# Kernel optimization log

Measured on AMD Instinct MI355X. Metric: run time of the kernel, lower is better.

## Reference

```python
import jax, jax.numpy as jnp
import numpy as np

B, C, H, W = 32, 384, 28, 28
E, HID, K = 4, 384, 2  # HID = hidden_features(1536) // num_experts(4)


def setup_inputs() -> dict:
    key = jax.random.key(0)
    ks = jax.random.split(key, 5)
    x = jax.random.normal(ks[0], (B, C, H, W), jnp.float32)
    gate_w = jax.random.normal(ks[1], (C, E), jnp.float32) * 0.02
    gate_b = jnp.zeros((E,), jnp.float32)
    w1 = jax.random.normal(ks[2], (E, HID, C), jnp.float32) * 0.02
    b1 = jnp.zeros((E, HID), jnp.float32)
    w2 = jax.random.normal(ks[3], (E, C, HID), jnp.float32) * 0.02
    b2 = jnp.zeros((E, C), jnp.float32)
    return {"x": x, "gate_w": gate_w, "gate_b": gate_b,
            "w1": w1, "b1": b1, "w2": w2, "b2": b2}


def reference(x, gate_w, gate_b, w1, b1, w2, b2):
    b, c, h, w = x.shape
    e = gate_b.shape[0]
    # per-token gating: tokens are spatial positions in NHWC order
    x_flat = x.transpose(0, 2, 3, 1).reshape(-1, c)          # [N, C], N = B*H*W
    scores = jax.nn.softmax(x_flat @ gate_w + gate_b, -1)    # [N, E]
    top_v, top_i = jax.lax.top_k(scores, K)                  # [N, K]
    top_w = jax.nn.softmax(top_v, -1)                        # [N, K] renormalized
    # weight map per top-k slot: [K, B, H, W]
    wmap = top_w.T.reshape(K, b, h, w)
    # faithful to torch loop: expert i contributes at slot k iff ANY token routed
    # to it at slot k; the weight applied is the UNMASKED slot-k weight map.
    present = (top_i[:, :, None] == jnp.arange(e)[None, None, :]).any(0)  # [K, E]
    coef = jnp.einsum('ke,kbhw->ebhw', present.astype(x.dtype), wmap)     # [E, B, H, W]
    # dense per-expert 1x1-conv MLP over the FULL tensor (as in the source)
    hdn = jax.nn.relu(jnp.einsum('bchw,edc->ebdhw', x, w1)
                      + b1[:, None, :, None, None])          # [E, B, HID, H, W]
    y = jnp.einsum('ebdhw,eod->ebohw', hdn, w2) + b2[:, None, :, None, None]
    out = jnp.einsum('ebohw,ebhw->bohw', y, coef)            # [B, C, H, W]
    return out
```

## Files before the change

### kernel.cpp

```cpp
#include <hip/hip_runtime.h>
#include <hip/hip_bf16.h>
#include <stdint.h>

#define B_DIM 32
#define C_DIM 384
#define HW_DIM 784
#define E_DIM 4
#define HID_DIM 384
#define NTOK (B_DIM * HW_DIM)
#define NH (E_DIM * HID_DIM)

using short8 = __attribute__((ext_vector_type(8))) short;
using f32x4  = __attribute__((ext_vector_type(4))) float;
typedef unsigned short ushort_t;

__device__ __forceinline__ ushort_t f2bf(float f) {
  __hip_bfloat16 h = __float2bfloat16(f);
  return __builtin_bit_cast(ushort_t, h);
}

__device__ __forceinline__ void gload_lds16(const void* g, void* l) {
  __builtin_amdgcn_global_load_lds(
      (const __attribute__((address_space(1))) unsigned int*)g,
      (__attribute__((address_space(3))) unsigned int*)l, 16, 0, 0);
}

__global__ __launch_bounds__(256) void prep_kernel(
    const float* __restrict__ w1, const float* __restrict__ w2,
    ushort_t* __restrict__ W1b, ushort_t* __restrict__ W2b,
    unsigned int* __restrict__ present) {
  int i = blockIdx.x * 256 + threadIdx.x;
  if (i == 0) *present = 0u;
  if (i < NH * C_DIM) {
    W1b[i] = f2bf(w1[i]);
    int o = i / NH;
    int r = i - o * NH;
    int e = r / HID_DIM;
    int k = r - e * HID_DIM;
    W2b[i] = f2bf(w2[((size_t)e * C_DIM + o) * HID_DIM + k]);
  }
}

__global__ __launch_bounds__(256) void gate_kernel(
    const float* __restrict__ x, const float* __restrict__ gw,
    const float* __restrict__ gb, ushort_t* __restrict__ xb,
    float* __restrict__ topw, unsigned int* __restrict__ present) {
  __shared__ __align__(16) ushort_t lxs[64][392];
  __shared__ float pscore[4][64][4];
  __shared__ unsigned int pmask;
  const int b = blockIdx.x;
  const int p0 = blockIdx.y * 64;
  const int cnt = min(64, HW_DIM - p0);
  const int tid = threadIdx.x;
  const int cg = tid >> 6, tl = tid & 63;
  if (tid == 0) pmask = 0u;
  float a0 = 0.f, a1 = 0.f, a2 = 0.f, a3 = 0.f;
  const bool valid = tl < cnt;
  if (valid) {
    const float* xp = x + (size_t)b * C_DIM * HW_DIM + p0 + tl;
    for (int c = cg; c < C_DIM; c += 4) {
      const float v = xp[(size_t)c * HW_DIM];
      lxs[tl][c] = f2bf(v);
      const float4 g = *(const float4*)&gw[c * 4];
      a0 += v * g.x; a1 += v * g.y; a2 += v * g.z; a3 += v * g.w;
    }
  }
  pscore[cg][tl][0] = a0; pscore[cg][tl][1] = a1;
  pscore[cg][tl][2] = a2; pscore[cg][tl][3] = a3;
  __syncthreads();
  if (cg == 0 && valid) {
    float z[4];
#pragma unroll
    for (int e = 0; e < 4; e++)
      z[e] = pscore[0][tl][e] + pscore[1][tl][e] + pscore[2][tl][e] +
             pscore[3][tl][e] + gb[e];
    const float mx = fmaxf(fmaxf(z[0], z[1]), fmaxf(z[2], z[3]));
    float s[4]; float sum = 0.f;
#pragma unroll
    for (int e = 0; e < 4; e++) { s[e] = __expf(z[e] - mx); sum += s[e]; }
    const float inv = 1.f / sum;
#pragma unroll
    for (int e = 0; e < 4; e++) s[e] *= inv;
    int e0 = 0; float v0 = s[0];
#pragma unroll
    for (int e = 1; e < 4; e++) if (s[e] > v0) { v0 = s[e]; e0 = e; }
    int e1 = -1; float v1 = -1.f;
#pragma unroll
    for (int e = 0; e < 4; e++) if (e != e0 && s[e] > v1) { v1 = s[e]; e1 = e; }
    const float r = __expf(v1 - v0);
    const float w0 = 1.f / (1.f + r);
    const int m = b * HW_DIM + p0 + tl;
    topw[m * 2] = w0;
    topw[m * 2 + 1] = 1.f - w0;
    atomicOr(&pmask, (1u << e0) | (1u << (4 + e1)));
  }
  __syncthreads();
  if (tid == 0) atomicOr(present, pmask);
  const int nchunk = cnt * 48;
  for (int ci = tid; ci < nchunk; ci += 256) {
    const int row = ci / 48, c8 = ci - row * 48;
    short8 v = *(const short8*)&lxs[row][c8 * 8];
    *(short8*)&xb[(size_t)(b * HW_DIM + p0 + row) * C_DIM + c8 * 8] = v;
  }
}

template <int KDIM, int EPI>
__global__ __launch_bounds__(256, 2) void gemm128(
    const ushort_t* __restrict__ A, const ushort_t* __restrict__ Bw,
    const float* __restrict__ bias, const float* __restrict__ topw,
    const unsigned int* __restrict__ presentp,
    ushort_t* __restrict__ hOut, float* __restrict__ outp) {
  constexpr int BM = 128, BN = 128, BK = 64;
  constexpr int KT = KDIM / BK;
  constexpr int NTN = (EPI == 0 ? NH / BN : C_DIM / BN);
  constexpr int ASZ = BM * BK;
  __shared__ ushort_t smem[4 * ASZ];

  const int nwg = NTN * (NTOK / BM);
  const int orig = blockIdx.x;
  const int xcd = orig & 7;
  const int qq = nwg >> 3, rr = nwg & 7;
  const int wg = (xcd < rr ? xcd * (qq + 1) : rr * (qq + 1) + (xcd - rr) * qq)
               + (orig >> 3);
  const int mt = wg / NTN, nt = wg % NTN;
  const int m0 = mt * BM, n0 = nt * BN;

  const int tid = threadIdx.x;
  const int lane = tid & 63;
  const int wid = tid >> 6;
  const int wm = wid >> 1, wn = wid & 1;

  auto stage = [&](int t) {
    ushort_t* dstA = smem + (t & 1) * ASZ;
    ushort_t* dstB = smem + 2 * ASZ + (t & 1) * ASZ;
    const int kb = t * BK;
#pragma unroll
    for (int li = 0; li < 4; ++li) {
      const int P = (li * 256 + tid) * 16;
      const int row = P >> 7;
      const int cb = (P & 127) ^ ((row & 7) << 4);
      gload_lds16(&A[(size_t)(m0 + row) * KDIM + kb + (cb >> 1)],
                  (char*)dstA + P);
    }
#pragma unroll
    for (int li = 0; li < 4; ++li) {
      const int P = (li * 256 + tid) * 16;
      const int row = P >> 7;
      const int cb = (P & 127) ^ ((row & 7) << 4);
      gload_lds16(&Bw[(size_t)(n0 + row) * KDIM + kb + (cb >> 1)],
                  (char*)dstB + P);
    }
  };

  f32x4 acc[4][4] = {};

  stage(0);
  stage(1);
  for (int t = 0; t < KT; ++t) {
    if (t + 1 < KT)
      asm volatile("s_waitcnt vmcnt(8)" ::: "memory");
    else
      asm volatile("s_waitcnt vmcnt(0)" ::: "memory");
    __builtin_amdgcn_sched_barrier(0);
    __builtin_amdgcn_s_barrier();
    __builtin_amdgcn_sched_barrier(0);
    const char* Ab = (const char*)(smem + (t & 1) * ASZ);
    const char* Bb = (const char*)(smem + 2 * ASZ + (t & 1) * ASZ);
    short8 av[4][2], bv[4][2];
#pragma unroll
    for (int i = 0; i < 4; ++i)
#pragma unroll
      for (int kk = 0; kk < 2; ++kk) {
        const int row = wm * 64 + i * 16 + (lane & 15);
        const int cb = (kk * 64 + ((lane >> 4) * 16)) ^ ((row & 7) << 4);
        av[i][kk] = *(const short8*)(Ab + row * 128 + cb);
      }
#pragma unroll
    for (int i = 0; i < 4; ++i)
#pragma unroll
      for (int kk = 0; kk < 2; ++kk) {
        const int row = wn * 64 + i * 16 + (lane & 15);
        const int cb = (kk * 64 + ((lane >> 4) * 16)) ^ ((row & 7) << 4);
        bv[i][kk] = *(const short8*)(Bb + row * 128 + cb);
      }
    __builtin_amdgcn_s_setprio(1);
#pragma unroll
    for (int kk = 0; kk < 2; ++kk)
#pragma unroll
      for (int i = 0; i < 4; ++i)
#pragma unroll
        for (int j = 0; j < 4; ++j)
          acc[i][j] = __builtin_amdgcn_mfma_f32_16x16x32_bf16(
              av[i][kk], bv[j][kk], acc[i][j], 0, 0, 0);
    __builtin_amdgcn_s_setprio(0);
    __builtin_amdgcn_sched_barrier(0);
    __builtin_amdgcn_s_barrier();
    __builtin_amdgcn_sched_barrier(0);
    if (t + 2 < KT) stage(t + 2);
  }

  const unsigned int pm = *presentp;
  if constexpr (EPI == 0) {
    ushort_t* tr = smem;
    const int e = n0 / HID_DIM;
    const float P0 = (float)((pm >> e) & 1u);
    const float P1 = (float)((pm >> (4 + e)) & 1u);
#pragma unroll
    for (int mi = 0; mi < 4; ++mi) {
      const int r0 = wm * 64 + mi * 16 + (lane >> 4) * 4;
      const int mg = m0 + r0;
      const float4 t0 = *(const float4*)&topw[mg * 2];
      const float4 t1 = *(const float4*)&topw[mg * 2 + 4];
      const float cj[4] = {P0 * t0.x + P1 * t0.y, P0 * t0.z + P1 * t0.w,
                           P0 * t1.x + P1 * t1.y, P0 * t1.z + P1 * t1.w};
#pragma unroll
      for (int ni = 0; ni < 4; ++ni) {
        const int cl = wn * 64 + ni * 16 + (lane & 15);
        const float bvv = bias[n0 + cl];
#pragma unroll
        for (int j = 0; j < 4; ++j) {
          float v = fmaxf(acc[mi][ni][j] + bvv, 0.f);
          tr[(r0 + j) * 128 + cl] = f2bf(cj[j] * v);
        }
      }
    }
    __syncthreads();
#pragma unroll
    for (int it = 0; it < 8; ++it) {
      const int c = it * 256 + tid;
      const int row = c >> 4, cr = c & 15;
      *(short8*)&hOut[(size_t)(m0 + row) * NH + n0 + cr * 8] =
          *(const short8*)&tr[row * 128 + cr * 8];
    }
  } else {
    float B0[4], B1[4];
#pragma unroll
    for (int ni = 0; ni < 4; ++ni) {
      const int o = n0 + wn * 64 + ni * 16 + (lane & 15);
      float s0 = 0.f, s1 = 0.f;
#pragma unroll
      for (int e2 = 0; e2 < 4; ++e2) {
        const float bb = bias[e2 * C_DIM + o];
        s0 += (float)((pm >> e2) & 1u) * bb;
        s1 += (float)((pm >> (4 + e2)) & 1u) * bb;
      }
      B0[ni] = s0; B1[ni] = s1;
    }
#pragma unroll
    for (int mi = 0; mi < 4; ++mi) {
      const int mg = m0 + wm * 64 + mi * 16 + (lane >> 4) * 4;
      const float4 t0 = *(const float4*)&topw[mg * 2];
      const float4 t1 = *(const float4*)&topw[mg * 2 + 4];
      const int bb2 = mg / HW_DIM;
      const int p = mg - bb2 * HW_DIM;
#pragma unroll
      for (int ni = 0; ni < 4; ++ni) {
        const int o = n0 + wn * 64 + ni * 16 + (lane & 15);
        float4 v;
        v.x = acc[mi][ni][0] + t0.x * B0[ni] + t0.y * B1[ni];
        v.y = acc[mi][ni][1] + t0.z * B0[ni] + t0.w * B1[ni];
        v.z = acc[mi][ni][2] + t1.x * B0[ni] + t1.y * B1[ni];
        v.w = acc[mi][ni][3] + t1.z * B0[ni] + t1.w * B1[ni];
        *(float4*)&outp[((size_t)bb2 * C_DIM + o) * HW_DIM + p] = v;
      }
    }
  }
}

extern "C" void kernel_launch(void* const* d_in, const int* in_sizes, int n_in,
                              void* d_out, int out_size, void* d_ws, size_t ws_size,
                              hipStream_t stream) {
  const float* x  = (const float*)d_in[0];
  const float* gw = (const float*)d_in[1];
  const float* gb = (const float*)d_in[2];
  const float* w1 = (const float*)d_in[3];
  const float* b1 = (const float*)d_in[4];
  const float* w2 = (const float*)d_in[5];
  const float* b2 = (const float*)d_in[6];
  float* out = (float*)d_out;

  char* ws = (char*)d_ws;
  ushort_t* xb = (ushort_t*)ws;   ws += (size_t)NTOK * C_DIM * 2;
  ushort_t* hdnS = (ushort_t*)ws; ws += (size_t)NTOK * NH * 2;
  ushort_t* W1b = (ushort_t*)ws;  ws += (size_t)NH * C_DIM * 2;
  ushort_t* W2b = (ushort_t*)ws;  ws += (size_t)C_DIM * NH * 2;
  float* topw = (float*)ws;       ws += (size_t)NTOK * 2 * 4;
  unsigned int* present = (unsigned int*)ws;

  prep_kernel<<<dim3((NH * C_DIM) / 256), dim3(256), 0, stream>>>(
      w1, w2, W1b, W2b, present);
  gate_kernel<<<dim3(B_DIM, 13), dim3(256), 0, stream>>>(
      x, gw, gb, xb, topw, present);
  gemm128<C_DIM, 0><<<dim3((NTOK / 128) * (NH / 128)), dim3(256), 0, stream>>>(
      xb, W1b, b1, topw, present, hdnS, nullptr);
  gemm128<NH, 1><<<dim3((NTOK / 128) * (C_DIM / 128)), dim3(256), 0, stream>>>(
      hdnS, W2b, b2, topw, present, nullptr, out);
}
```

Before: 130.2 us.

## Split GEMM main loop into four interleaved LDS-read/MFMA quadrant phases

Splits the per-tile K-step of the bf16 MFMA GEMM into four quadrant phases, each loading only the A/B fragments it needs from LDS and then issuing MFMAs, with barriers between phases. The next tile's global-to-LDS stage is issued before the last quadrant's MFMAs so global loads overlap compute. It also precomputes the swizzled LDS row and column offsets once outside the loop. The extra barriers per K-step add sync overhead, and a __syncthreads is added before the epilogue reuses shared memory.

Result: no change. 130.6 us (+0.3%).

```diff
diff --git a/kernel.cpp b/kernel.cpp
--- a/kernel.cpp
+++ b/kernel.cpp
@@ -154,6 +154,11 @@
 
   f32x4 acc[4][4] = {};
 
+  const int rA = wm * 64 + (lane & 15);
+  const int rB = wn * 64 + (lane & 15);
+  const int cb0 = ((lane >> 4) * 16) ^ ((lane & 7) << 4);
+  const int cb1 = (64 + (lane >> 4) * 16) ^ ((lane & 7) << 4);
+
   stage(0);
   stage(1);
   for (int t = 0; t < KT; ++t) {
@@ -164,43 +169,93 @@
     __builtin_amdgcn_sched_barrier(0);
     __builtin_amdgcn_s_barrier();
     __builtin_amdgcn_sched_barrier(0);
-    const char* Ab = (const char*)(smem + (t & 1) * ASZ);
-    const char* Bb = (const char*)(smem + 2 * ASZ + (t & 1) * ASZ);
+    const char* Ab = (const char*)(smem + (t & 1) * ASZ) + rA * 128;
+    const char* Bb = (const char*)(smem + 2 * ASZ + (t & 1) * ASZ) + rB * 128;
     short8 av[4][2], bv[4][2];
-#pragma unroll
-    for (int i = 0; i < 4; ++i)
-#pragma unroll
-      for (int kk = 0; kk < 2; ++kk) {
-        const int row = wm * 64 + i * 16 + (lane & 15);
-        const int cb = (kk * 64 + ((lane >> 4) * 16)) ^ ((row & 7) << 4);
-        av[i][kk] = *(const short8*)(Ab + row * 128 + cb);
-      }
-#pragma unroll
-    for (int i = 0; i < 4; ++i)
-#pragma unroll
-      for (int kk = 0; kk < 2; ++kk) {
-        const int row = wn * 64 + i * 16 + (lane & 15);
-        const int cb = (kk * 64 + ((lane >> 4) * 16)) ^ ((row & 7) << 4);
-        bv[i][kk] = *(const short8*)(Bb + row * 128 + cb);
-      }
+
+#pragma unroll
+    for (int i = 0; i < 2; ++i) {
+      av[i][0] = *(const short8*)(Ab + i * 2048 + cb0);
+      av[i][1] = *(const short8*)(Ab + i * 2048 + cb1);
+      bv[i][0] = *(const short8*)(Bb + i * 2048 + cb0);
+      bv[i][1] = *(const short8*)(Bb + i * 2048 + cb1);
+    }
+    __builtin_amdgcn_sched_barrier(0);
+    __builtin_amdgcn_s_barrier();
     __builtin_amdgcn_s_setprio(1);
 #pragma unroll
     for (int kk = 0; kk < 2; ++kk)
 #pragma unroll
-      for (int i = 0; i < 4; ++i)
-#pragma unroll
-        for (int j = 0; j < 4; ++j)
+      for (int i = 0; i < 2; ++i)
+#pragma unroll
+        for (int j = 0; j < 2; ++j)
           acc[i][j] = __builtin_amdgcn_mfma_f32_16x16x32_bf16(
               av[i][kk], bv[j][kk], acc[i][j], 0, 0, 0);
     __builtin_amdgcn_s_setprio(0);
     __builtin_amdgcn_sched_barrier(0);
     __builtin_amdgcn_s_barrier();
     __builtin_amdgcn_sched_barrier(0);
+
+#pragma unroll
+    for (int i = 2; i < 4; ++i) {
+      bv[i][0] = *(const short8*)(Bb + i * 2048 + cb0);
+      bv[i][1] = *(const short8*)(Bb + i * 2048 + cb1);
+    }
+    __builtin_amdgcn_sched_barrier(0);
+    __builtin_amdgcn_s_barrier();
+    __builtin_amdgcn_s_setprio(1);
+#pragma unroll
+    for (int kk = 0; kk < 2; ++kk)
+#pragma unroll
+      for (int i = 0; i < 2; ++i)
+#pragma unroll
+        for (int j = 2; j < 4; ++j)
+          acc[i][j] = __builtin_amdgcn_mfma_f32_16x16x32_bf16(
+              av[i][kk], bv[j][kk], acc[i][j], 0, 0, 0);
+    __builtin_amdgcn_s_setprio(0);
+    __builtin_amdgcn_sched_barrier(0);
+    __builtin_amdgcn_s_barrier();
+    __builtin_amdgcn_sched_barrier(0);
+
+#pragma unroll
+    for (int i = 2; i < 4; ++i) {
+      av[i][0] = *(const short8*)(Ab + i * 2048 + cb0);
+      av[i][1] = *(const short8*)(Ab + i * 2048 + cb1);
+    }
+    __builtin_amdgcn_sched_barrier(0);
+    __builtin_amdgcn_s_barrier();
+    __builtin_amdgcn_s_setprio(1);
+#pragma unroll
+    for (int kk = 0; kk < 2; ++kk)
+#pragma unroll
+      for (int i = 2; i < 4; ++i)
+#pragma unroll
+        for (int j = 2; j < 4; ++j)
+          acc[i][j] = __builtin_amdgcn_mfma_f32_16x16x32_bf16(
+              av[i][kk], bv[j][kk], acc[i][j], 0, 0, 0);
+    __builtin_amdgcn_s_setprio(0);
+    __builtin_amdgcn_sched_barrier(0);
+    __builtin_amdgcn_s_barrier();
+    __builtin_amdgcn_sched_barrier(0);
+
     if (t + 2 < KT) stage(t + 2);
+    __builtin_amdgcn_sched_barrier(0);
+    __builtin_amdgcn_s_setprio(1);
+#pragma unroll
+    for (int kk = 0; kk < 2; ++kk)
+#pragma unroll
+      for (int i = 2; i < 4; ++i)
+#pragma unroll
+        for (int j = 0; j < 2; ++j)
+          acc[i][j] = __builtin_amdgcn_mfma_f32_16x16x32_bf16(
+              av[i][kk], bv[j][kk], acc[i][j], 0, 0, 0);
+    __builtin_amdgcn_s_setprio(0);
+    __builtin_amdgcn_sched_barrier(0);
   }
 
   const unsigned int pm = *presentp;
   if constexpr (EPI == 0) {
+    __syncthreads();
     ushort_t* tr = smem;
     const int e = n0 / HID_DIM;
     const float P0 = (float)((pm >> e) & 1u);
```

## Use 256x256 tiles with 8-wave quadrant-pipelined schedule for first expert GEMM

Applied to the files above, without the earlier changes.

The first GEMM (tokens x 1536 hidden) moves from a 128x128 tile with 4 waves to a 256x256 tile with 8 waves and 128KB of LDS. Loads are split into half-tiles that are staged while MFMA quadrants run, in a ping-pong-style fine-grained schedule. The aim is more operand reuse per byte loaded and better overlap of global-to-LDS loads with compute. The costs are heavy LDS use that limits occupancy to one block per CU, more barriers, a per-column expert lookup in the epilogue, and a wave tail since 588 tiles do not split evenly across the CUs. The second GEMM is unchanged apart from being separated out of the template.

Measured after the change: 138.7 us. +6.5%, slower.

```diff
diff --git a/kernel.cpp b/kernel.cpp
--- a/kernel.cpp
+++ b/kernel.cpp
@@ -104,31 +104,212 @@
   }
 }
 
-template <int KDIM, int EPI>
-__global__ __launch_bounds__(256, 2) void gemm128(
+__global__ __launch_bounds__(512, 2) void moe_g1(
     const ushort_t* __restrict__ A, const ushort_t* __restrict__ Bw,
     const float* __restrict__ bias, const float* __restrict__ topw,
-    const unsigned int* __restrict__ presentp,
-    ushort_t* __restrict__ hOut, float* __restrict__ outp) {
-  constexpr int BM = 128, BN = 128, BK = 64;
+    const unsigned int* __restrict__ presentp, ushort_t* __restrict__ hOut) {
+  constexpr int KT = 6;
+  __shared__ __align__(16) char smemb[131072];
+
+  const int nwg = 98 * 6;
+  const int orig = blockIdx.x;
+  const int xcd = orig & 7;
+  const int qq = nwg >> 3, rr = nwg & 7;
+  const int wg = (xcd < rr ? xcd * (qq + 1) : rr * (qq + 1) + (xcd - rr) * qq)
+               + (orig >> 3);
+  const int mt = wg / 6, nt = wg % 6;
+  const int m0 = mt * 256, n0 = nt * 256;
+
+  const int tid = threadIdx.x;
+  const int lane = tid & 63;
+  const int wid = tid >> 6;
+  const int wm = wid >> 2, wn = wid & 3;
+  const int lanel = lane & 15, laneq = lane >> 4;
+  const int swz = (lanel & 7) << 4;
+
+  auto AOFF = [](int b, int h) { return b * 32768 + h * 16384; };
+  auto BOFF = [](int b, int h) { return 65536 + b * 32768 + h * 16384; };
+
+  auto stage = [&](int mat, int tau, int h) {
+    const int base = (mat == 0 ? AOFF(tau & 1, h) : BOFF(tau & 1, h));
+#pragma unroll
+    for (int li = 0; li < 2; ++li) {
+      const int P = (li * 512 + tid) * 16;
+      const int r128 = P >> 7;
+      const int cb = P & 127;
+      const int k = tau * 64 + (((cb) ^ ((r128 & 7) << 4)) >> 1);
+      if (mat == 0) {
+        const int grow = m0 + (r128 >> 6) * 128 + h * 64 + (r128 & 63);
+        gload_lds16(&A[(size_t)grow * C_DIM + k], smemb + base + P);
+      } else {
+        const int gcol = n0 + (r128 >> 5) * 64 + h * 32 + (r128 & 31);
+        gload_lds16(&Bw[(size_t)gcol * C_DIM + k], smemb + base + P);
+      }
+    }
+  };
+
+  f32x4 acc[8][4] = {};
+  short8 av[4][2], bv0[2][2], bv1[2][2];
+
+  auto read_av = [&](int buf, int qm) {
+#pragma unroll
+    for (int mi = 0; mi < 4; ++mi)
+#pragma unroll
+      for (int kk = 0; kk < 2; ++kk) {
+        const int r128 = wm * 64 + mi * 16 + lanel;
+        av[mi][kk] = *(const short8*)(smemb + AOFF(buf, qm) + r128 * 128 +
+                                      ((kk * 64 + laneq * 16) ^ swz));
+      }
+  };
+  auto read_bv = [&](int buf, int qn, short8 (*bv)[2]) {
+#pragma unroll
+    for (int ni = 0; ni < 2; ++ni)
+#pragma unroll
+      for (int kk = 0; kk < 2; ++kk) {
+        const int c128 = wn * 32 + ni * 16 + lanel;
+        bv[ni][kk] = *(const short8*)(smemb + BOFF(buf, qn) + c128 * 128 +
+                                      ((kk * 64 + laneq * 16) ^ swz));
+      }
+  };
+
+#define SB() __builtin_amdgcn_sched_barrier(0)
+#define BAR() do { SB(); __builtin_amdgcn_s_barrier(); SB(); } while (0)
+#define LGKM0() do { asm volatile("s_waitcnt lgkmcnt(0)" ::: "memory"); SB(); } while (0)
+#define MFMA_Q(qm, qn, BV)                                             \
+  do {                                                                 \
+    __builtin_amdgcn_s_setprio(1);                                     \
+    _Pragma("unroll") for (int kk = 0; kk < 2; ++kk)                   \
+    _Pragma("unroll") for (int mi = 0; mi < 4; ++mi)                   \
+    _Pragma("unroll") for (int ni = 0; ni < 2; ++ni)                   \
+      acc[(qm)*4 + mi][(qn)*2 + ni] =                                  \
+          __builtin_amdgcn_mfma_f32_16x16x32_bf16(                     \
+              av[mi][kk], BV[ni][kk], acc[(qm)*4 + mi][(qn)*2 + ni],   \
+              0, 0, 0);                                                \
+    __builtin_amdgcn_s_setprio(0);                                     \
+  } while (0)
+
+  stage(0, 0, 0); stage(1, 0, 0); stage(1, 0, 1); stage(0, 0, 1);
+  stage(0, 1, 0); stage(1, 1, 0); stage(1, 1, 1); stage(0, 1, 1);
+
+#pragma unroll
+  for (int it2 = 0; it2 < KT / 2; ++it2) {
+    const int T = 2 * it2;
+    if (it2 > 0) stage(0, T + 1, 1);
+    asm volatile("s_waitcnt vmcnt(8)" ::: "memory");
+    BAR();
+    read_av(0, 0); read_bv(0, 0, bv0);
+    LGKM0();
+    MFMA_Q(0, 0, bv0);
+    BAR();
+    read_bv(0, 1, bv1);
+    if (T + 2 < KT) stage(0, T + 2, 0);
+    BAR();
+    LGKM0();
+    MFMA_Q(0, 1, bv1);
+    BAR();
+    read_av(0, 1);
+    if (T + 2 < KT) stage(1, T + 2, 0);
+    BAR();
+    LGKM0();
+    MFMA_Q(1, 0, bv0);
+    BAR();
+    if (T + 2 < KT) stage(1, T + 2, 1);
+    BAR();
+    MFMA_Q(1, 1, bv1);
+    BAR();
+    if (T + 2 < KT) stage(0, T + 2, 1);
+    if (T + 2 < KT)
+      asm volatile("s_waitcnt vmcnt(8)" ::: "memory");
+    else
+      asm volatile("s_waitcnt vmcnt(0)" ::: "memory");
+    BAR();
+    read_av(1, 0); read_bv(1, 0, bv0);
+    LGKM0();
+    MFMA_Q(0, 0, bv0);
+    BAR();
+    read_bv(1, 1, bv1);
+    if (T + 3 < KT) stage(0, T + 3, 0);
+    BAR();
+    LGKM0();
+    MFMA_Q(0, 1, bv1);
+    BAR();
+    read_av(1, 1);
+    if (T + 3 < KT) stage(1, T + 3, 0);
+    BAR();
+    LGKM0();
+    MFMA_Q(1, 0, bv0);
+    BAR();
+    if (T + 3 < KT) stage(1, T + 3, 1);
+    BAR();
+    MFMA_Q(1, 1, bv1);
+    BAR();
+  }
+
+  const unsigned int pm = *presentp;
+  __syncthreads();
+#pragma unroll
+  for (int mi = 0; mi < 8; ++mi) {
+    const int r0 = wm * 128 + mi * 16 + laneq * 4;
+    const int mg = m0 + r0;
+    const float4 t0 = *(const float4*)&topw[mg * 2];
+    const float4 t1 = *(const float4*)&topw[mg * 2 + 4];
+#pragma unroll
+    for (int ni = 0; ni < 4; ++ni) {
+      const int cl = wn * 64 + ni * 16 + lanel;
+      const int e = (n0 + cl) / HID_DIM;
+      const float P0e = (float)((pm >> e) & 1u);
+      const float P1e = (float)((pm >> (4 + e)) & 1u);
+      const float bvv = bias[n0 + cl];
+      const float cj[4] = {P0e * t0.x + P1e * t0.y, P0e * t0.z + P1e * t0.w,
+                           P0e * t1.x + P1e * t1.y, P0e * t1.z + P1e * t1.w};
+#pragma unroll
+      for (int j = 0; j < 4; ++j) {
+        const int rr = r0 + j;
+        float v = fmaxf(acc[mi][ni][j] + bvv, 0.f);
+        *(ushort_t*)(smemb + rr * 512 + ((cl * 2) ^ ((rr & 7) << 4))) =
+            f2bf(cj[j] * v);
+      }
+    }
+  }
+  __syncthreads();
+#pragma unroll
+  for (int it = 0; it < 16; ++it) {
+    const int c = it * 512 + tid;
+    const int row = c >> 5, c8 = c & 31;
+    short8 v = *(const short8*)(smemb + row * 512 +
+                                ((c8 * 16) ^ ((row & 7) << 4)));
+    *(short8*)&hOut[(size_t)(m0 + row) * NH + n0 + c8 * 8] = v;
+  }
+#undef SB
+#undef BAR
+#undef LGKM0
+#undef MFMA_Q
+}
+
+__global__ __launch_bounds__(256, 2) void gemm2_k(
+    const ushort_t* __restrict__ A, const ushort_t* __restrict__ Bw,
+    const float* __restrict__ bias, const float* __restrict__ topw,
+    const unsigned int* __restrict__ presentp, float* __restrict__ outp) {
+  constexpr int KDIM = NH, BK = 64;
   constexpr int KT = KDIM / BK;
-  constexpr int NTN = (EPI == 0 ? NH / BN : C_DIM / BN);
-  constexpr int ASZ = BM * BK;
+  constexpr int NTN = C_DIM / 128;
+  constexpr int ASZ = 128 * BK;
   __shared__ ushort_t smem[4 * ASZ];
 
-  const int nwg = NTN * (NTOK / BM);
+  const int nwg = NTN * (NTOK / 128);
   const int orig = blockIdx.x;
   const int xcd = orig & 7;
   const int qq = nwg >> 3, rr = nwg & 7;
   const int wg = (xcd < rr ? xcd * (qq + 1) : rr * (qq + 1) + (xcd - rr) * qq)
                + (orig >> 3);
   const int mt = wg / NTN, nt = wg % NTN;
-  const int m0 = mt * BM, n0 = nt * BN;
+  const int m0 = mt * 128, n0 = nt * 128;
 
   const int tid = threadIdx.x;
   const int lane = tid & 63;
   const int wid = tid >> 6;
   const int wm = wid >> 1, wn = wid & 1;
+  const int lanel = lane & 15, laneq = lane >> 4;
 
   auto stage = [&](int t) {
     ushort_t* dstA = smem + (t & 1) * ASZ;
@@ -171,16 +352,16 @@
     for (int i = 0; i < 4; ++i)
 #pragma unroll
       for (int kk = 0; kk < 2; ++kk) {
-        const int row = wm * 64 + i * 16 + (lane & 15);
-        const int cb = (kk * 64 + ((lane >> 4) * 16)) ^ ((row & 7) << 4);
+        const int row = wm * 64 + i * 16 + lanel;
+        const int cb = (kk * 64 + (laneq * 16)) ^ ((row & 7) << 4);
         av[i][kk] = *(const short8*)(Ab + row * 128 + cb);
       }
 #pragma unroll
     for (int i = 0; i < 4; ++i)
 #pragma unroll
       for (int kk = 0; kk < 2; ++kk) {
-        const int row = wn * 64 + i * 16 + (lane & 15);
-        const int cb = (kk * 64 + ((lane >> 4) * 16)) ^ ((row & 7) << 4);
+        const int row = wn * 64 + i * 16 + lanel;
+        const int cb = (kk * 64 + (laneq * 16)) ^ ((row & 7) << 4);
         bv[i][kk] = *(const short8*)(Bb + row * 128 + cb);
       }
     __builtin_amdgcn_s_setprio(1);
@@ -200,69 +381,35 @@
   }
 
   const unsigned int pm = *presentp;
-  if constexpr (EPI == 0) {
-    ushort_t* tr = smem;
-    const int e = n0 / HID_DIM;
-    const float P0 = (float)((pm >> e) & 1u);
-    const float P1 = (float)((pm >> (4 + e)) & 1u);
-#pragma unroll
-    for (int mi = 0; mi < 4; ++mi) {
-      const int r0 = wm * 64 + mi * 16 + (lane >> 4) * 4;
-      const int mg = m0 + r0;
-      const float4 t0 = *(const float4*)&topw[mg * 2];
-      const float4 t1 = *(const float4*)&topw[mg * 2 + 4];
-      const float cj[4] = {P0 * t0.x + P1 * t0.y, P0 * t0.z + P1 * t0.w,
-                           P0 * t1.x + P1 * t1.y, P0 * t1.z + P1 * t1.w};
-#pragma unroll
-      for (int ni = 0; ni < 4; ++ni) {
-        const int cl = wn * 64 + ni * 16 + (lane & 15);
-        const float bvv = bias[n0 + cl];
-#pragma unroll
-        for (int j = 0; j < 4; ++j) {
-          float v = fmaxf(acc[mi][ni][j] + bvv, 0.f);
-          tr[(r0 + j) * 128 + cl] = f2bf(cj[j] * v);
-        }
-      }
-    }
-    __syncthreads();
-#pragma unroll
-    for (int it = 0; it < 8; ++it) {
-      const int c = it * 256 + tid;
-      const int row = c >> 4, cr = c & 15;
-      *(short8*)&hOut[(size_t)(m0 + row) * NH + n0 + cr * 8] =
-          *(const short8*)&tr[row * 128 + cr * 8];
-    }
-  } else {
-    float B0[4], B1[4];
+  float B0[4], B1[4];
+#pragma unroll
+  for (int ni = 0; ni < 4; ++ni) {
+    const int o = n0 + wn * 64 + ni * 16 + lanel;
+    float s0 = 0.f, s1 = 0.f;
+#pragma unroll
+    for (int e2 = 0; e2 < 4; ++e2) {
+      const float bb = bias[e2 * C_DIM + o];
+      s0 += (float)((pm >> e2) & 1u) * bb;
+      s1 += (float)((pm >> (4 + e2)) & 1u) * bb;
+    }
+    B0[ni] = s0; B1[ni] = s1;
+  }
+#pragma unroll
+  for (int mi = 0; mi < 4; ++mi) {
+    const int mg = m0 + wm * 64 + mi * 16 + laneq * 4;
+    const float4 t0 = *(const float4*)&topw[mg * 2];
+    const float4 t1 = *(const float4*)&topw[mg * 2 + 4];
+    const int bb2 = mg / HW_DIM;
+    const int p = mg - bb2 * HW_DIM;
 #pragma unroll
     for (int ni = 0; ni < 4; ++ni) {
-      const int o = n0 + wn * 64 + ni * 16 + (lane & 15);
-      float s0 = 0.f, s1 = 0.f;
-#pragma unroll
-      for (int e2 = 0; e2 < 4; ++e2) {
-        const float bb = bias[e2 * C_DIM + o];
-        s0 += (float)((pm >> e2) & 1u) * bb;
-        s1 += (float)((pm >> (4 + e2)) & 1u) * bb;
-      }
-      B0[ni] = s0; B1[ni] = s1;
-    }
-#pragma unroll
-    for (int mi = 0; mi < 4; ++mi) {
-      const int mg = m0 + wm * 64 + mi * 16 + (lane >> 4) * 4;
-      const float4 t0 = *(const float4*)&topw[mg * 2];
-      const float4 t1 = *(const float4*)&topw[mg * 2 + 4];
-      const int bb2 = mg / HW_DIM;
-      const int p = mg - bb2 * HW_DIM;
-#pragma unroll
-      for (int ni = 0; ni < 4; ++ni) {
-        const int o = n0 + wn * 64 + ni * 16 + (lane & 15);
-        float4 v;
-        v.x = acc[mi][ni][0] + t0.x * B0[ni] + t0.y * B1[ni];
-        v.y = acc[mi][ni][1] + t0.z * B0[ni] + t0.w * B1[ni];
-        v.z = acc[mi][ni][2] + t1.x * B0[ni] + t1.y * B1[ni];
-        v.w = acc[mi][ni][3] + t1.z * B0[ni] + t1.w * B1[ni];
-        *(float4*)&outp[((size_t)bb2 * C_DIM + o) * HW_DIM + p] = v;
-      }
+      const int o = n0 + wn * 64 + ni * 16 + lanel;
+      float4 v;
+      v.x = acc[mi][ni][0] + t0.x * B0[ni] + t0.y * B1[ni];
+      v.y = acc[mi][ni][1] + t0.z * B0[ni] + t0.w * B1[ni];
+      v.z = acc[mi][ni][2] + t1.x * B0[ni] + t1.y * B1[ni];
+      v.w = acc[mi][ni][3] + t1.z * B0[ni] + t1.w * B1[ni];
+      *(float4*)&outp[((size_t)bb2 * C_DIM + o) * HW_DIM + p] = v;
     }
   }
 }
@@ -291,8 +438,8 @@
       w1, w2, W1b, W2b, present);
   gate_kernel<<<dim3(B_DIM, 13), dim3(256), 0, stream>>>(
       x, gw, gb, xb, topw, present);
-  gemm128<C_DIM, 0><<<dim3((NTOK / 128) * (NH / 128)), dim3(256), 0, stream>>>(
-      xb, W1b, b1, topw, present, hdnS, nullptr);
-  gemm128<NH, 1><<<dim3((NTOK / 128) * (C_DIM / 128)), dim3(256), 0, stream>>>(
-      hdnS, W2b, b2, topw, present, nullptr, out);
-}
+  moe_g1<<<dim3((NTOK / 256) * (NH / 256)), dim3(512), 0, stream>>>(
+      xb, W1b, b1, topw, present, hdnS);
+  gemm2_k<<<dim3((NTOK / 128) * (C_DIM / 128)), dim3(256), 0, stream>>>(
+      hdnS, W2b, b2, topw, present, out);
+}
```
